# Kernel tuning notes

Measured on AMD Instinct MI355X. Metric: run time of the kernel, lower is better.

The kernel has to match this reference:

```python
import jax, jax.numpy as jnp
import numpy as np

B_LARGE, B_SMALL = 256, 256
R_LARGE, R_SMALL = 64, 16
N_LARGE, N_SMALL = 128, 128
D = 4096


def setup_inputs() -> dict:
    key = jax.random.key(0)
    k1, k2, k3, k4, k5 = jax.random.split(key, 5)
    x = jax.random.normal(k1, (B_LARGE + B_SMALL, 1, D), dtype=jnp.float16)
    wids_large = jax.random.randint(k2, (B_LARGE,), 0, N_LARGE, dtype=jnp.int32)
    wids_small = jax.random.randint(k3, (B_SMALL,), 0, N_SMALL, dtype=jnp.int32)
    lora_A_large = (jax.random.normal(k4, (N_LARGE, D, R_LARGE), dtype=jnp.float16) * jnp.float16(0.02))
    lora_A_small = (jax.random.normal(k5, (N_SMALL, D, R_SMALL), dtype=jnp.float16) * jnp.float16(0.02))
    return {"x": x, "wids_large": wids_large, "wids_small": wids_small,
            "lora_A_large": lora_A_large, "lora_A_small": lora_A_small}


def reference(x, wids_large, wids_small, lora_A_large, lora_A_small):
    # split batch into large / small adapter groups
    x_l = x[:B_LARGE]          # [Bl, 1, D]
    x_s = x[B_LARGE:]          # [Bs, 1, D]
    # gather per-sample adapter matrices, then batched matmul (BGMV pattern)
    A_l = lora_A_large[wids_large]   # [Bl, D, r_large]
    A_s = lora_A_small[wids_small]   # [Bs, D, r_small]
    y_large = jnp.einsum('bsd,bdr->bsr', x_l, A_l)  # [Bl, 1, r_large]
    y_small = jnp.einsum('bsd,bdr->bsr', x_s, A_s)  # [Bs, 1, r_small]
    return (y_large, y_small)
```

## Files before the change

kernel.cpp:

```cpp
#include <hip/hip_runtime.h>

#define NDIM 4096
#define B_LG 256
#define B_SM 256
#define N_WID 128
#define R_LG 64
#define R_SM 16
#define BLOCK 512
#define MAXB 256
#define MAXM 6
#define PF 8
#define OUT_SIZE (B_LG * R_LG + B_SM * R_SM)

#define DCH_LG 512
#define NCH_LG 4
#define DCH_SM 1024
#define NCH_SM 4
#define GRID_MAIN 512

typedef float floatv4 __attribute__((ext_vector_type(4)));

#define WS_NWORK  0
#define WS_BKT_L  256
#define WS_BKT_S  (WS_BKT_L + N_WID * MAXB)
#define WS_WORK   (WS_BKT_S + N_WID * MAXB)

__global__ __launch_bounds__(BLOCK)
void setup_kernel(const int* __restrict__ wids_l,
                  const int* __restrict__ wids_s,
                  int* __restrict__ ws,
                  float* __restrict__ out)
{
    __shared__ int cl[N_WID], cs[N_WID];
    __shared__ int nwork;
    const int t = threadIdx.x;
    if (t < N_WID) { cl[t] = 0; cs[t] = 0; }
    if (t == 0) nwork = 0;
    __syncthreads();
    if (t < B_LG) {
        const int w = wids_l[t];
        const int s = atomicAdd(&cl[w], 1);
        ws[WS_BKT_L + w * MAXB + s] = t;
    } else if (t < B_LG + B_SM) {
        const int b = t - B_LG;
        const int w = wids_s[b];
        const int s = atomicAdd(&cs[w], 1);
        ws[WS_BKT_S + w * MAXB + s] = b;
    }
    __syncthreads();
    if (t < N_WID) {
        int cnt = cl[t];
        for (int g = 0; g < cnt; g += MAXM) {
            const int Mi   = min(MAXM, cnt - g);
            const int base = atomicAdd(&nwork, 2);
            for (int h = 0; h < 2; ++h) {
                ws[WS_WORK + 2 * (base + h)]     = (t << 8) | h;
                ws[WS_WORK + 2 * (base + h) + 1] = (g << 8) | Mi;
            }
        }
        cnt = cs[t];
        for (int g = 0; g < cnt; g += MAXM) {
            const int Mi   = min(MAXM, cnt - g);
            const int base = atomicAdd(&nwork, 1);
            ws[WS_WORK + 2 * base]     = (1 << 30) | (t << 8);
            ws[WS_WORK + 2 * base + 1] = (g << 8) | Mi;
        }
    }
    __syncthreads();
    if (t == 0) ws[WS_NWORK] = nwork;
    for (int i = t; i < OUT_SIZE; i += BLOCK) out[i] = 0.0f;
}

template<int R, int M, int DCH, int NCH>
__device__ __forceinline__ void gemv_item(
    const float* __restrict__ x,
    const float* __restrict__ Ab,
    float* __restrict__ outb,
    const int* __restrict__ batches,
    int dbase,
    float* __restrict__ xs,
    float* __restrict__ red)
{
    constexpr int LPR  = R / 4;
    constexpr int ROWS = BLOCK / LPR;
    constexpr int IT   = DCH / ROWS;
    constexpr int NG   = IT / PF;
    static_assert(IT % PF == 0, "chunk not divisible by pipeline group");

    const int t = threadIdx.x;

    int rows[M];
#pragma unroll
    for (int m = 0; m < M; ++m) rows[m] = batches[m];

    const int d_sub  = t / LPR;
    const int r_base = (t % LPR) * 4;

    float acc[M][4];
#pragma unroll
    for (int m = 0; m < M; ++m)
#pragma unroll
        for (int j = 0; j < 4; ++j) acc[m][j] = 0.0f;

    for (int c = 0; c < NCH; ++c) {
        const int d0 = dbase + c * DCH;

        __syncthreads();
#pragma unroll
        for (int m = 0; m < M; ++m)
            for (int i = t; i < DCH / 4; i += BLOCK)
                reinterpret_cast<float4*>(xs + m * DCH)[i] =
                    reinterpret_cast<const float4*>(x + (size_t)rows[m] * NDIM + d0)[i];
        __syncthreads();

        const float* Abt = Ab + ((size_t)d0 + d_sub) * R + r_base;

#pragma unroll
        for (int g = 0; g < NG; ++g) {
            floatv4 buf[PF];
#pragma unroll
            for (int p = 0; p < PF; ++p)
                buf[p] = __builtin_nontemporal_load(
                    reinterpret_cast<const floatv4*>(Abt + (size_t)(g * PF + p) * ROWS * R));
#pragma unroll
            for (int p = 0; p < PF; ++p) {
                const int d = (g * PF + p) * ROWS + d_sub;
#pragma unroll
                for (int m = 0; m < M; ++m) {
                    const float xv = xs[m * DCH + d];
                    acc[m][0] = fmaf(xv, buf[p].x, acc[m][0]);
                    acc[m][1] = fmaf(xv, buf[p].y, acc[m][1]);
                    acc[m][2] = fmaf(xv, buf[p].z, acc[m][2]);
                    acc[m][3] = fmaf(xv, buf[p].w, acc[m][3]);
                }
            }
        }
    }

    const int wave = t >> 6;
    const int lane = t & 63;
#pragma unroll
    for (int m = 0; m < M; ++m)
#pragma unroll
        for (int off = 32; off >= LPR; off >>= 1)
#pragma unroll
            for (int j = 0; j < 4; ++j)
                acc[m][j] += __shfl_down(acc[m][j], off, 64);

#pragma unroll
    for (int m = 0; m < M; ++m) {
        __syncthreads();
        if (lane < LPR)
#pragma unroll
            for (int j = 0; j < 4; ++j) red[(wave * 16 + lane) * 4 + j] = acc[m][j];
        __syncthreads();
        if (t < R) {
            const int rl = t / 4, j = t % 4;
            float v = 0.0f;
#pragma unroll
            for (int w = 0; w < 8; ++w) v += red[(w * 16 + rl) * 4 + j];
            atomicAdd(outb + (size_t)rows[m] * R + t, v);
        }
    }
}

__global__ __launch_bounds__(BLOCK, 4)
void SequentialLoraA_kernel(const float* __restrict__ x,
                            const float* __restrict__ Al,
                            const float* __restrict__ As,
                            float* __restrict__ out,
                            const int* __restrict__ ws)
{
    __shared__ float xs[MAXM * DCH_SM];
    __shared__ float red[8 * 16 * 4];

    const int it = blockIdx.x;
    if (it >= ws[WS_NWORK]) return;

    const int a   = ws[WS_WORK + 2 * it];
    const int b   = ws[WS_WORK + 2 * it + 1];
    const int wid = (a >> 8) & 0x7f;
    const int Mi  = b & 0xff;
    const int gs  = b >> 8;

    if (a & (1 << 30)) {
        const float* xb  = x + (size_t)B_LG * NDIM;
        const float* Ab  = As + (size_t)wid * NDIM * R_SM;
        float*       ob  = out + (size_t)B_LG * R_LG;
        const int*   bkt = ws + WS_BKT_S + wid * MAXB + gs;
        switch (Mi) {
          case 1:  gemv_item<R_SM, 1, DCH_SM, NCH_SM>(xb, Ab, ob, bkt, 0, xs, red); break;
          case 2:  gemv_item<R_SM, 2, DCH_SM, NCH_SM>(xb, Ab, ob, bkt, 0, xs, red); break;
          case 3:  gemv_item<R_SM, 3, DCH_SM, NCH_SM>(xb, Ab, ob, bkt, 0, xs, red); break;
          case 4:  gemv_item<R_SM, 4, DCH_SM, NCH_SM>(xb, Ab, ob, bkt, 0, xs, red); break;
          case 5:  gemv_item<R_SM, 5, DCH_SM, NCH_SM>(xb, Ab, ob, bkt, 0, xs, red); break;
          default: gemv_item<R_SM, 6, DCH_SM, NCH_SM>(xb, Ab, ob, bkt, 0, xs, red); break;
        }
    } else {
        const int dbase = (a & 1) * (NCH_LG * DCH_LG);
        const float* Ab  = Al + (size_t)wid * NDIM * R_LG;
        const int*   bkt = ws + WS_BKT_L + wid * MAXB + gs;
        switch (Mi) {
          case 1:  gemv_item<R_LG, 1, DCH_LG, NCH_LG>(x, Ab, out, bkt, dbase, xs, red); break;
          case 2:  gemv_item<R_LG, 2, DCH_LG, NCH_LG>(x, Ab, out, bkt, dbase, xs, red); break;
          case 3:  gemv_item<R_LG, 3, DCH_LG, NCH_LG>(x, Ab, out, bkt, dbase, xs, red); break;
          case 4:  gemv_item<R_LG, 4, DCH_LG, NCH_LG>(x, Ab, out, bkt, dbase, xs, red); break;
          case 5:  gemv_item<R_LG, 5, DCH_LG, NCH_LG>(x, Ab, out, bkt, dbase, xs, red); break;
          default: gemv_item<R_LG, 6, DCH_LG, NCH_LG>(x, Ab, out, bkt, dbase, xs, red); break;
        }
    }
}

extern "C" void kernel_launch(void* const* d_in, const int* in_sizes, int n_in,
                              void* d_out, int out_size, void* d_ws, size_t ws_size,
                              hipStream_t stream) {
    const float* x      = (const float*)d_in[0];
    const int*   wids_l = (const int*)d_in[1];
    const int*   wids_s = (const int*)d_in[2];
    const float* Al     = (const float*)d_in[3];
    const float* As     = (const float*)d_in[4];
    float* out = (float*)d_out;
    int*   ws  = (int*)d_ws;

    setup_kernel<<<1, BLOCK, 0, stream>>>(wids_l, wids_s, ws, out);
    SequentialLoraA_kernel<<<GRID_MAIN, BLOCK, 0, stream>>>(x, Al, As, out, ws);
}
```

Baseline: 216.5 us.

## Use persistent blocks with atomic ticket work queue and finer D-split items

Replaces the one-block-per-item grid with persistent blocks that fetch work items through a global atomic ticket counter. Large-rank items now split D into four quarters instead of two halves. Small-rank items group up to four samples and stage the full x row in shared memory at once. The aim is better load balance and fewer per-chunk barriers. In exchange it adds more atomicAdd traffic on the output, a larger shared-memory footprint (64KB for xs) that may reduce occupancy, and serialized ticket atomics.

```diff
diff --git a/kernel.cpp b/kernel.cpp
--- a/kernel.cpp
+++ b/kernel.cpp
@@ -8,19 +8,19 @@
 #define R_SM 16
 #define BLOCK 512
 #define MAXB 256
-#define MAXM 6
+#define MAXM_LG 6
+#define MAXM_SM 4
 #define PF 8
 #define OUT_SIZE (B_LG * R_LG + B_SM * R_SM)
 
-#define DCH_LG 512
-#define NCH_LG 4
-#define DCH_SM 1024
-#define NCH_SM 4
+#define DCH_LG 1024
+#define DCH_SM 4096
 #define GRID_MAIN 512
 
 typedef float floatv4 __attribute__((ext_vector_type(4)));
 
 #define WS_NWORK  0
+#define WS_TICKET 1
 #define WS_BKT_L  256
 #define WS_BKT_S  (WS_BKT_L + N_WID * MAXB)
 #define WS_WORK   (WS_BKT_S + N_WID * MAXB)
@@ -50,28 +50,28 @@
     __syncthreads();
     if (t < N_WID) {
         int cnt = cl[t];
-        for (int g = 0; g < cnt; g += MAXM) {
-            const int Mi   = min(MAXM, cnt - g);
-            const int base = atomicAdd(&nwork, 2);
-            for (int h = 0; h < 2; ++h) {
-                ws[WS_WORK + 2 * (base + h)]     = (t << 8) | h;
-                ws[WS_WORK + 2 * (base + h) + 1] = (g << 8) | Mi;
+        for (int g = 0; g < cnt; g += MAXM_LG) {
+            const int Mi   = min(MAXM_LG, cnt - g);
+            const int base = atomicAdd(&nwork, 4);
+            for (int q = 0; q < 4; ++q) {
+                ws[WS_WORK + 2 * (base + q)]     = (t << 8) | q;
+                ws[WS_WORK + 2 * (base + q) + 1] = (g << 8) | Mi;
             }
         }
         cnt = cs[t];
-        for (int g = 0; g < cnt; g += MAXM) {
-            const int Mi   = min(MAXM, cnt - g);
+        for (int g = 0; g < cnt; g += MAXM_SM) {
+            const int Mi   = min(MAXM_SM, cnt - g);
             const int base = atomicAdd(&nwork, 1);
             ws[WS_WORK + 2 * base]     = (1 << 30) | (t << 8);
             ws[WS_WORK + 2 * base + 1] = (g << 8) | Mi;
         }
     }
     __syncthreads();
-    if (t == 0) ws[WS_NWORK] = nwork;
+    if (t == 0) { ws[WS_NWORK] = nwork; ws[WS_TICKET] = 0; }
     for (int i = t; i < OUT_SIZE; i += BLOCK) out[i] = 0.0f;
 }
 
-template<int R, int M, int DCH, int NCH>
+template<int R, int M, int DCH>
 __device__ __forceinline__ void gemv_item(
     const float* __restrict__ x,
     const float* __restrict__ Ab,
@@ -85,16 +85,24 @@
     constexpr int ROWS = BLOCK / LPR;
     constexpr int IT   = DCH / ROWS;
     constexpr int NG   = IT / PF;
-    static_assert(IT % PF == 0, "chunk not divisible by pipeline group");
+    static_assert(IT % PF == 0, "item not divisible by pipeline group");
 
     const int t = threadIdx.x;
 
     int rows[M];
 #pragma unroll
     for (int m = 0; m < M; ++m) rows[m] = batches[m];
+
+#pragma unroll
+    for (int m = 0; m < M; ++m)
+        for (int i = t; i < DCH / 4; i += BLOCK)
+            reinterpret_cast<float4*>(xs + m * DCH)[i] =
+                reinterpret_cast<const float4*>(x + (size_t)rows[m] * NDIM + dbase)[i];
+    __syncthreads();
 
     const int d_sub  = t / LPR;
     const int r_base = (t % LPR) * 4;
+    const float* Abt = Ab + ((size_t)dbase + d_sub) * R + r_base;
 
     float acc[M][4];
 #pragma unroll
@@ -102,37 +110,23 @@
 #pragma unroll
         for (int j = 0; j < 4; ++j) acc[m][j] = 0.0f;
 
-    for (int c = 0; c < NCH; ++c) {
-        const int d0 = dbase + c * DCH;
-
-        __syncthreads();
-#pragma unroll
-        for (int m = 0; m < M; ++m)
-            for (int i = t; i < DCH / 4; i += BLOCK)
-                reinterpret_cast<float4*>(xs + m * DCH)[i] =
-                    reinterpret_cast<const float4*>(x + (size_t)rows[m] * NDIM + d0)[i];
-        __syncthreads();
-
-        const float* Abt = Ab + ((size_t)d0 + d_sub) * R + r_base;
-
-#pragma unroll
-        for (int g = 0; g < NG; ++g) {
-            floatv4 buf[PF];
-#pragma unroll
-            for (int p = 0; p < PF; ++p)
-                buf[p] = __builtin_nontemporal_load(
-                    reinterpret_cast<const floatv4*>(Abt + (size_t)(g * PF + p) * ROWS * R));
-#pragma unroll
-            for (int p = 0; p < PF; ++p) {
-                const int d = (g * PF + p) * ROWS + d_sub;
-#pragma unroll
-                for (int m = 0; m < M; ++m) {
-                    const float xv = xs[m * DCH + d];
-                    acc[m][0] = fmaf(xv, buf[p].x, acc[m][0]);
-                    acc[m][1] = fmaf(xv, buf[p].y, acc[m][1]);
-                    acc[m][2] = fmaf(xv, buf[p].z, acc[m][2]);
-                    acc[m][3] = fmaf(xv, buf[p].w, acc[m][3]);
-                }
+#pragma unroll
+    for (int g = 0; g < NG; ++g) {
+        floatv4 buf[PF];
+#pragma unroll
+        for (int p = 0; p < PF; ++p)
+            buf[p] = __builtin_nontemporal_load(
+                reinterpret_cast<const floatv4*>(Abt + (size_t)(g * PF + p) * ROWS * R));
+#pragma unroll
+        for (int p = 0; p < PF; ++p) {
+            const int d = (g * PF + p) * ROWS + d_sub;
+#pragma unroll
+            for (int m = 0; m < M; ++m) {
+                const float xv = xs[m * DCH + d];
+                acc[m][0] = fmaf(xv, buf[p].x, acc[m][0]);
+                acc[m][1] = fmaf(xv, buf[p].y, acc[m][1]);
+                acc[m][2] = fmaf(xv, buf[p].z, acc[m][2]);
+                acc[m][3] = fmaf(xv, buf[p].w, acc[m][3]);
             }
         }
     }
@@ -169,44 +163,51 @@
                             const float* __restrict__ Al,
                             const float* __restrict__ As,
                             float* __restrict__ out,
-                            const int* __restrict__ ws)
+                            int* __restrict__ ws)
 {
-    __shared__ float xs[MAXM * DCH_SM];
+    __shared__ float xs[MAXM_SM * DCH_SM];
     __shared__ float red[8 * 16 * 4];
-
-    const int it = blockIdx.x;
-    if (it >= ws[WS_NWORK]) return;
-
-    const int a   = ws[WS_WORK + 2 * it];
-    const int b   = ws[WS_WORK + 2 * it + 1];
-    const int wid = (a >> 8) & 0x7f;
-    const int Mi  = b & 0xff;
-    const int gs  = b >> 8;
-
-    if (a & (1 << 30)) {
-        const float* xb  = x + (size_t)B_LG * NDIM;
-        const float* Ab  = As + (size_t)wid * NDIM * R_SM;
-        float*       ob  = out + (size_t)B_LG * R_LG;
-        const int*   bkt = ws + WS_BKT_S + wid * MAXB + gs;
-        switch (Mi) {
-          case 1:  gemv_item<R_SM, 1, DCH_SM, NCH_SM>(xb, Ab, ob, bkt, 0, xs, red); break;
-          case 2:  gemv_item<R_SM, 2, DCH_SM, NCH_SM>(xb, Ab, ob, bkt, 0, xs, red); break;
-          case 3:  gemv_item<R_SM, 3, DCH_SM, NCH_SM>(xb, Ab, ob, bkt, 0, xs, red); break;
-          case 4:  gemv_item<R_SM, 4, DCH_SM, NCH_SM>(xb, Ab, ob, bkt, 0, xs, red); break;
-          case 5:  gemv_item<R_SM, 5, DCH_SM, NCH_SM>(xb, Ab, ob, bkt, 0, xs, red); break;
-          default: gemv_item<R_SM, 6, DCH_SM, NCH_SM>(xb, Ab, ob, bkt, 0, xs, red); break;
-        }
-    } else {
-        const int dbase = (a & 1) * (NCH_LG * DCH_LG);
-        const float* Ab  = Al + (size_t)wid * NDIM * R_LG;
-        const int*   bkt = ws + WS_BKT_L + wid * MAXB + gs;
-        switch (Mi) {
-          case 1:  gemv_item<R_LG, 1, DCH_LG, NCH_LG>(x, Ab, out, bkt, dbase, xs, red); break;
-          case 2:  gemv_item<R_LG, 2, DCH_LG, NCH_LG>(x, Ab, out, bkt, dbase, xs, red); break;
-          case 3:  gemv_item<R_LG, 3, DCH_LG, NCH_LG>(x, Ab, out, bkt, dbase, xs, red); break;
-          case 4:  gemv_item<R_LG, 4, DCH_LG, NCH_LG>(x, Ab, out, bkt, dbase, xs, red); break;
-          case 5:  gemv_item<R_LG, 5, DCH_LG, NCH_LG>(x, Ab, out, bkt, dbase, xs, red); break;
-          default: gemv_item<R_LG, 6, DCH_LG, NCH_LG>(x, Ab, out, bkt, dbase, xs, red); break;
+    __shared__ int s_item;
+
+    const int t  = threadIdx.x;
+    const int nw = ws[WS_NWORK];
+
+    for (;;) {
+        __syncthreads();
+        if (t == 0) s_item = atomicAdd(ws + WS_TICKET, 1);
+        __syncthreads();
+        const int it = s_item;
+        if (it >= nw) return;
+
+        const int a   = ws[WS_WORK + 2 * it];
+        const int b   = ws[WS_WORK + 2 * it + 1];
+        const int wid = (a >> 8) & 0x7f;
+        const int Mi  = b & 0xff;
+        const int gs  = b >> 8;
+
+        if (a & (1 << 30)) {
+            const float* xb  = x + (size_t)B_LG * NDIM;
+            const float* Ab  = As + (size_t)wid * NDIM * R_SM;
+            float*       ob  = out + (size_t)B_LG * R_LG;
+            const int*   bkt = ws + WS_BKT_S + wid * MAXB + gs;
+            switch (Mi) {
+              case 1:  gemv_item<R_SM, 1, DCH_SM>(xb, Ab, ob, bkt, 0, xs, red); break;
+              case 2:  gemv_item<R_SM, 2, DCH_SM>(xb, Ab, ob, bkt, 0, xs, red); break;
+              case 3:  gemv_item<R_SM, 3, DCH_SM>(xb, Ab, ob, bkt, 0, xs, red); break;
+              default: gemv_item<R_SM, 4, DCH_SM>(xb, Ab, ob, bkt, 0, xs, red); break;
+            }
+        } else {
+            const int dbase = (a & 0xff) * DCH_LG;
+            const float* Ab  = Al + (size_t)wid * NDIM * R_LG;
+            const int*   bkt = ws + WS_BKT_L + wid * MAXB + gs;
+            switch (Mi) {
+              case 1:  gemv_item<R_LG, 1, DCH_LG>(x, Ab, out, bkt, dbase, xs, red); break;
+              case 2:  gemv_item<R_LG, 2, DCH_LG>(x, Ab, out, bkt, dbase, xs, red); break;
+              case 3:  gemv_item<R_LG, 3, DCH_LG>(x, Ab, out, bkt, dbase, xs, red); break;
+              case 4:  gemv_item<R_LG, 4, DCH_LG>(x, Ab, out, bkt, dbase, xs, red); break;
+              case 5:  gemv_item<R_LG, 5, DCH_LG>(x, Ab, out, bkt, dbase, xs, red); break;
+              default: gemv_item<R_LG, 6, DCH_LG>(x, Ab, out, bkt, dbase, xs, red); break;
+            }
         }
     }
 }
```

Measured after the change: 233.7 us. 1.08x slower.
